# Kernel tuning notes

Hardware: AMD Instinct MI355X
Metric: run time of the kernel (lower is better)

## Reference

```python
import jax, jax.numpy as jnp
import numpy as np

B, N, FN, FE, OUT = 64, 128, 64, 16, 128
S, VOCAB, EMB, LH = 1033, 1033, 50, 8
MOMO, SIDE, T = 200, 963, 3
LN_EPS, BN_EPS = 1e-12, 1e-5


def setup_inputs():
    key = jax.random.key(0)
    ks = iter(jax.random.split(key, 64))
    def nrm(shape, scale=0.05):
        return jax.random.normal(next(ks), shape, dtype=jnp.float32) * scale
    inp = {}
    inp['adjacency_1'] = (jax.random.uniform(next(ks), (B, N, N)) < 0.1).astype(jnp.float32)
    inp['nodes_1'] = nrm((B, N, FN), 1.0)
    inp['edges_1'] = nrm((B, N, N, FE), 1.0)
    inp['adjacency_2'] = (jax.random.uniform(next(ks), (B, N, N)) < 0.1).astype(jnp.float32)
    inp['nodes_2'] = nrm((B, N, FN), 1.0)
    inp['edges_2'] = nrm((B, N, N, FE), 1.0)
    inp['d1_momo_fts'] = nrm((B, MOMO), 1.0)
    inp['d2_momo_fts'] = nrm((B, MOMO), 1.0)
    inp['d1_protein_fts'] = jax.random.randint(next(ks), (B, S), 0, VOCAB)
    inp['d2_protein_fts'] = jax.random.randint(next(ks), (B, S), 0, VOCAB)
    inp['side_effect'] = nrm((B, SIDE), 1.0)
    inp['word_emb'] = nrm((VOCAB, EMB))
    inp['pos_emb'] = nrm((VOCAB, EMB))
    inp['ln_gamma'] = jnp.ones((EMB,), jnp.float32)
    inp['ln_beta'] = jnp.zeros((EMB,), jnp.float32)
    inp['W_ih'] = nrm((4 * LH, EMB))
    inp['W_hh'] = nrm((4 * LH, LH))
    inp['b_ih'] = jnp.zeros((4 * LH,), jnp.float32)
    inp['b_hh'] = jnp.zeros((4 * LH,), jnp.float32)
    inp['dec_W1'] = nrm((LH * S, 256))
    inp['dec_b1'] = jnp.zeros((256,), jnp.float32)
    inp['bn_gamma'] = jnp.ones((256,), jnp.float32)
    inp['bn_beta'] = jnp.zeros((256,), jnp.float32)
    inp['dec_W2'] = nrm((256, 45))
    inp['dec_b2'] = jnp.zeros((45,), jnp.float32)
    for g in ('1', '2'):
        inp['W_msg' + g] = nrm((FN, FN))
        inp['W_edge' + g] = nrm((FE, FN))
        inp['W_up' + g] = nrm((2 * FN, FN))
        inp['b_up' + g] = jnp.zeros((FN,), jnp.float32)
        inp['W_read' + g] = nrm((2 * FN, OUT))
        inp['b_read' + g] = jnp.zeros((OUT,), jnp.float32)
    inp['W_momo'] = nrm((MOMO, 45))
    inp['b_momo'] = jnp.zeros((45,), jnp.float32)
    inp['W_side'] = nrm((SIDE, 32))
    inp['b_side'] = jnp.zeros((32,), jnp.float32)
    inp['W_final'] = nrm((2 * (OUT + 45 + 45) + 32, 1))
    inp['b_final'] = jnp.zeros((1,), jnp.float32)
    return inp


def _mpnn(adj, nodes, edges, W_msg, W_edge, W_up, b_up, W_read, b_read):
    # Dense-masked equivalent of the padded neighbor/edge gather construction:
    # message[b,n] = sum_m adj[b,n,m] * (h[b,m] @ W_msg + e[b,n,m] @ W_edge)
    node_mask = adj.sum(-1) > 0  # [B,N] -- only connected nodes are updated
    edge_msg = jnp.einsum('bnm,bnmf,fk->bnk', adj, edges, W_edge)  # static over passes
    h = nodes
    for _ in range(T):
        msg = jnp.einsum('bnm,bmf,fk->bnk', adj, h, W_msg) + edge_msg
        upd = jax.nn.relu(jnp.concatenate([h, msg], -1) @ W_up + b_up)
        h = jnp.where(node_mask[..., None], upd, h)
    r = jax.nn.relu(jnp.concatenate([h, nodes], -1) @ W_read + b_read)  # [B,N,OUT]
    return jnp.einsum('bn,bnk->bk', node_mask.astype(h.dtype), r)


def _protein(ids, word_emb, pos_emb, ln_gamma, ln_beta, W_ih, W_hh, b_ih, b_hh,
             dec_W1, dec_b1, bn_gamma, bn_beta, dec_W2, dec_b2):
    x = word_emb[ids] + pos_emb[jnp.arange(S)][None]  # [B,S,EMB]
    u = x.mean(-1, keepdims=True)
    s = ((x - u) ** 2).mean(-1, keepdims=True)
    x = ln_gamma * (x - u) / jnp.sqrt(s + LN_EPS) + ln_beta
    def step(carry, xt):  # torch LSTM gate order: i, f, g, o
        h, c = carry
        gates = xt @ W_ih.T + b_ih + h @ W_hh.T + b_hh
        i, f, g, o = jnp.split(gates, 4, axis=-1)
        c = jax.nn.sigmoid(f) * c + jax.nn.sigmoid(i) * jnp.tanh(g)
        h = jax.nn.sigmoid(o) * jnp.tanh(c)
        return (h, c), h
    h0 = jnp.zeros((ids.shape[0], LH), jnp.float32)
    _, hs = jax.lax.scan(step, (h0, h0), jnp.swapaxes(x, 0, 1))  # [S,B,LH]
    p = jnp.swapaxes(hs, 0, 1).reshape(ids.shape[0], -1)  # [B, S*LH]
    p = jax.nn.relu(p @ dec_W1 + dec_b1)
    m, v = p.mean(0), p.var(0)  # BatchNorm1d in training mode (batch stats)
    p = bn_gamma * (p - m) / jnp.sqrt(v + BN_EPS) + bn_beta
    return p @ dec_W2 + dec_b2  # [B,45]


def reference(adjacency_1, nodes_1, edges_1, adjacency_2, nodes_2, edges_2,
              d1_momo_fts, d1_protein_fts, d2_momo_fts, d2_protein_fts, side_effect,
              word_emb, pos_emb, ln_gamma, ln_beta, W_ih, W_hh, b_ih, b_hh,
              dec_W1, dec_b1, bn_gamma, bn_beta, dec_W2, dec_b2,
              W_msg1, W_edge1, W_up1, b_up1, W_read1, b_read1,
              W_msg2, W_edge2, W_up2, b_up2, W_read2, b_read2,
              W_momo, b_momo, W_side, b_side, W_final, b_final):
    out1 = _mpnn(adjacency_1, nodes_1, edges_1, W_msg1, W_edge1, W_up1, b_up1, W_read1, b_read1)
    out2 = _mpnn(adjacency_2, nodes_2, edges_2, W_msg2, W_edge2, W_up2, b_up2, W_read2, b_read2)
    p1 = _protein(d1_protein_fts, word_emb, pos_emb, ln_gamma, ln_beta, W_ih, W_hh, b_ih, b_hh,
                  dec_W1, dec_b1, bn_gamma, bn_beta, dec_W2, dec_b2)
    p2 = _protein(d2_protein_fts, word_emb, pos_emb, ln_gamma, ln_beta, W_ih, W_hh, b_ih, b_hh,
                  dec_W1, dec_b1, bn_gamma, bn_beta, dec_W2, dec_b2)
    momo1 = d1_momo_fts @ W_momo + b_momo
    momo2 = d2_momo_fts @ W_momo + b_momo
    drug1 = jnp.concatenate([out1, p1, momo1], axis=1)
    drug2 = jnp.concatenate([out2, p2, momo2], axis=1)
    side = side_effect @ W_side + b_side
    feats = jnp.concatenate([drug1, drug2, side], axis=1)
    return feats @ W_final + b_final  # [B,1]
```

## Files before the change

kernel.cpp:

```cpp
#include <hip/hip_runtime.h>
#include <hip/hip_bf16.h>
#include <math.h>

#define Bb 64
#define Nn 128
#define FNf 64
#define Ss 1033
#define EMBe 50

typedef float f4 __attribute__((ext_vector_type(4)));
typedef float f2 __attribute__((ext_vector_type(2)));
typedef int   i4 __attribute__((ext_vector_type(4)));

#define HS_KSTRIDE 1036
#define HS_BSTRIDE 8288
#define HS_PSIZE   530432

constexpr size_t OFF_EMSG  = 2*524288 + 2*524288;
constexpr size_t OFF_MASK  = OFF_EMSG  + 2*524288;
constexpr size_t OFF_OUT12 = OFF_MASK  + 2*8192;
constexpr size_t OFF_PPRE  = OFF_OUT12 + 2*8192;
constexpr size_t OFF_PBN   = OFF_PPRE  + 2*16384;
constexpr size_t OFF_XW    = OFF_PBN   + 2*16384;
constexpr size_t OFF_HS    = OFF_XW    + 2*2115584;
constexpr size_t OFF_W2F   = OFF_HS    + 2*HS_PSIZE;
constexpr size_t OFF_WMF   = OFF_W2F   + 2*256;
constexpr size_t OFF_WSF   = OFF_WMF   + 2*200;
constexpr size_t OFF_CONST = OFF_WSF   + 964;
constexpr size_t OFF_COUNT = OFF_CONST + 4;
constexpr size_t OFF_NZ    = OFF_COUNT + 2*8192;
constexpr size_t OFF_AVAL  = OFF_NZ    + 2*524288;

__device__ inline f4 relu4(f4 v) {
  v[0] = fmaxf(v[0], 0.f); v[1] = fmaxf(v[1], 0.f);
  v[2] = fmaxf(v[2], 0.f); v[3] = fmaxf(v[3], 0.f);
  return v;
}

#define ROR16(x, n) __int_as_float(__builtin_amdgcn_update_dpp(0, __float_as_int(x), 0x120 + (n), 0xF, 0xF, true))

__global__ __launch_bounds__(256) void kA(
    const float* __restrict__ adj1, const float* __restrict__ adj2,
    const float* __restrict__ edges1, const float* __restrict__ edges2,
    const float* __restrict__ We1, const float* __restrict__ We2,
    const int* __restrict__ ids1, const int* __restrict__ ids2,
    const float* __restrict__ we, const float* __restrict__ pe,
    const float* __restrict__ lng, const float* __restrict__ lnb,
    const float* __restrict__ Wih, const float* __restrict__ bih,
    const float* __restrict__ bhh, float* __restrict__ ws) {
  int bid = blockIdx.x;
  int t = threadIdx.x;
  if (bid < 4096) {
    int g = bid >> 11;
    int w = t >> 6, lane = t & 63;
    int row = (bid & 2047) * 4 + w;
    const float* adj   = g ? adj2 : adj1;
    const float* edges = g ? edges2 : edges1;
    const float* We    = g ? We2 : We1;
    float* emsg  = ws + OFF_EMSG + (size_t)g * 524288;
    int*   cntg  = (int*)(ws + OFF_COUNT) + (size_t)g * 8192;
    int*   nz    = (int*)(ws + OFF_NZ)    + (size_t)g * 524288;
    float* aval  = ws + OFF_AVAL + (size_t)g * 524288;

    __shared__ int   lidx[4][64];
    __shared__ float lav[4][64];
    __shared__ float les[4][16];

    const float* arow = adj + (size_t)row * 128;
    float a0 = arow[lane], a1 = arow[64 + lane];
    unsigned long long m0 = __ballot(a0 != 0.f);
    unsigned long long m1 = __ballot(a1 != 0.f);
    int c0 = __popcll(m0);
    int cnt = c0 + __popcll(m1);
    unsigned long long below = ((unsigned long long)1 << lane) - 1ull;
    if (a0 != 0.f) { int pos = __popcll(m0 & below); if (pos < 64) { lidx[w][pos] = lane; lav[w][pos] = a0; } }
    if (a1 != 0.f) { int pos = c0 + __popcll(m1 & below); if (pos < 64) { lidx[w][pos] = lane + 64; lav[w][pos] = a1; } }
    int cc = cnt > 64 ? 64 : cnt;
    __syncthreads();

    nz[(size_t)row * 64 + lane]   = (lane < cc) ? lidx[w][lane] : 0;
    aval[(size_t)row * 64 + lane] = (lane < cc) ? lav[w][lane] : 0.f;

    int f = lane & 15, js = lane >> 4;
    float es = 0.f;
    const float* erow = edges + (size_t)row * 128 * 16;
    for (int j = js; j < cc; j += 4) es += lav[w][j] * erow[lidx[w][j] * 16 + f];
    es += __shfl_xor(es, 16);
    es += __shfl_xor(es, 32);
    if (lane < 16) les[w][lane] = es;
    __syncthreads();

    float acc = 0.f;
    #pragma unroll
    for (int ff = 0; ff < 16; ++ff) acc += les[w][ff] * We[ff * 64 + lane];
    emsg[(size_t)row * 64 + lane] = acc;
    if (lane == 0) cntg[row] = cc;
    return;
  }
  int bid6 = bid - 4096;
  int p = bid6 / 2066;
  int xb = bid6 % 2066;
  const int* ids = p ? ids2 : ids1;
  float* xw = ws + OFF_XW + (size_t)p * 2115584;
  __shared__ float wlds[1600];
  __shared__ float glds[50], blds[50], bs[32];
  __shared__ float xl6[8][52];
  for (int i = t; i < 1600; i += 256) wlds[i] = Wih[i];
  if (t < 50) { glds[t] = lng[t]; blds[t] = lnb[t]; }
  if (t < 32) bs[t] = bih[t] + bhh[t];
  __syncthreads();
  int grp = t >> 5, tl = t & 31;
  int newpos = (tl < 16) ? 2 * tl : 2 * tl - 31;
  const float L = 1.44269504088896f;
  float scale = (tl >= 16 && tl < 24) ? -2.f * L : -L;
  int q0 = xb * 32 + grp * 4;
  for (int qq = 0; qq < 4; ++qq) {
    int q = q0 + qq;
    int s = q % Ss;
    int id = ids[q];
    const float* wr = we + (size_t)id * 50;
    const float* pr = pe + (size_t)s * 50;
    float x1 = wr[tl] + pr[tl];
    bool has2 = (tl + 32) < 50;
    float x2 = has2 ? (wr[tl + 32] + pr[tl + 32]) : 0.f;
    float sm = x1 + x2, sq = x1 * x1 + x2 * x2;
    #pragma unroll
    for (int off = 16; off; off >>= 1) {
      sm += __shfl_xor(sm, off, 32);
      sq += __shfl_xor(sq, off, 32);
    }
    float u = sm * (1.f / 50.f);
    float var = fmaxf(sq * (1.f / 50.f) - u * u, 0.f);
    float rstd = rsqrtf(var + 1e-12f);
    xl6[grp][tl] = glds[tl] * (x1 - u) * rstd + blds[tl];
    if (has2) xl6[grp][tl + 32] = glds[tl + 32] * (x2 - u) * rstd + blds[tl + 32];
    __syncthreads();
    float acc = bs[tl];
    #pragma unroll 10
    for (int k = 0; k < 50; ++k) acc += xl6[grp][k] * wlds[tl * 50 + k];
    xw[(size_t)q * 32 + newpos] = acc * scale;
    __syncthreads();
  }
}

__global__ __launch_bounds__(256) void kB(
    const float* __restrict__ nodes1, const float* __restrict__ nodes2,
    const float* __restrict__ Wm1, const float* __restrict__ Wm2,
    const float* __restrict__ Wup1, const float* __restrict__ Wup2,
    const float* __restrict__ bup1, const float* __restrict__ bup2,
    const float* __restrict__ Wr1, const float* __restrict__ Wr2,
    const float* __restrict__ br1, const float* __restrict__ br2,
    const float* __restrict__ Whh, float* __restrict__ ws) {
  __shared__ __attribute__((aligned(16))) float hl[8192];
  __shared__ __attribute__((aligned(16))) float xl[8192];
  __shared__ __attribute__((aligned(16))) float wml[4096];
  __shared__ __attribute__((aligned(16))) float wbl[8192];
  int bid = blockIdx.x;
  int t = threadIdx.x;
  if (bid >= 128) {
    if (t >= 64) return;
    int idx = bid - 128;
    int p = idx >> 4, xb = idx & 15;
    const float* xw = ws + OFF_XW + (size_t)p * 2115584;
    float* hs = ws + OFF_HS + (size_t)p * HS_PSIZE;
    int lane16 = t & 15;
    int k = lane16 & 7;
    int half = lane16 >> 3;
    int b = xb * 4 + (t >> 4);
    const float* xwp = xw + (size_t)b * (Ss * 32) + lane16 * 2;
    float* hq = hs + (size_t)b * HS_BSTRIDE + (size_t)k * HS_KSTRIDE;
    const float L = 1.44269504088896f;
    int ga = half ? 8 + k : k;
    int gb = half ? 24 + k : 16 + k;
    float sb_scale = half ? -L : -2.f * L;
    float wa[8], wb[8];
    #pragma unroll
    for (int r = 0; r < 8; ++r) {
      int j = (k - r) & 7;
      wa[r] = -L * Whh[ga * 8 + j];
      wb[r] = sb_scale * Whh[gb * 8 + j];
    }
    float A = half ? 0.f : -4.f * L;
    float B = half ? 1.f : 2.f * L;
    float ho = 0.f, cs = 0.f;
    float q0v = 0.f, q1v = 0.f, q2v = 0.f, q3v = 0.f;

    f2 x[8];
    #pragma unroll
    for (int j = 0; j < 8; ++j) x[j] = *(const f2*)(xwp + (size_t)j * 32);
    const float* pf = xwp + 8 * 32;

    auto step = [&](f2 xc) {
      float h1 = ROR16(ho, 1);
      float h2 = ROR16(ho, 2);
      float h3 = ROR16(ho, 3);
      float h4 = ROR16(ho, 4);
      float h5 = ROR16(ho, 5);
      float h6 = ROR16(ho, 6);
      float h7 = ROR16(ho, 7);
      float a0 = fmaf(ho, wa[0], xc.x);
      float b0 = fmaf(ho, wb[0], xc.y);
      a0 = fmaf(h1, wa[1], a0);  b0 = fmaf(h1, wb[1], b0);
      a0 = fmaf(h2, wa[2], a0);  b0 = fmaf(h2, wb[2], b0);
      a0 = fmaf(h3, wa[3], a0);  b0 = fmaf(h3, wb[3], b0);
      float a1 = h4 * wa[4];     float b1 = h4 * wb[4];
      a1 = fmaf(h5, wa[5], a1);  b1 = fmaf(h5, wb[5], b1);
      a1 = fmaf(h6, wa[6], a1);  b1 = fmaf(h6, wb[6], b1);
      a1 = fmaf(h7, wa[7], a1);  b1 = fmaf(h7, wb[7], b1);
      float acc_a = a0 + a1;
      float acc_b = b0 + b1;
      float ea = __builtin_amdgcn_exp2f(acc_a);
      float sa = __builtin_amdgcn_rcpf(1.f + ea);
      float eb = __builtin_amdgcn_exp2f(acc_b);
      float tb = __builtin_amdgcn_rcpf(1.f + eb);
      float x_own = fmaf(sa * A, tb, sa * B);
      float x_oth = ROR16(x_own, 8);
      float t_oth = ROR16(tb, 8);
      float F  = half ? x_own : x_oth;
      float P2 = half ? x_oth : x_own;
      cs = fmaf(F, cs, P2);
      float e2 = __builtin_amdgcn_exp2f(cs);
      float tc = __builtin_amdgcn_rcpf(1.f + e2);
      float so = half ? tb : t_oth;
      ho = fmaf(so + so, tc, -so);
    };

    for (int g = 0; g < 129; ++g) {
      #pragma unroll
      for (int j = 0; j < 8; ++j) {
        f2 xc = x[j];
        x[j] = *(const f2*)(pf + j * 32);
        step(xc);
        if (j == 0 || j == 4) q0v = ho;
        else if (j == 1 || j == 5) q1v = ho;
        else if (j == 2 || j == 6) q2v = ho;
        else if (j == 3) { q3v = ho; if (!half) *(f4*)(hq + 0) = (f4){q0v, q1v, q2v, q3v}; }
        else { q3v = ho; if (!half) *(f4*)(hq + 4) = (f4){q0v, q1v, q2v, q3v}; }
      }
      pf += 256;
      hq += 8;
    }
    step(x[0]);
    if (!half) hq[0] = ho;
    return;
  }
  int g = bid >> 6, b = bid & 63;
  const float* nodes = g ? nodes2 : nodes1;
  const float* Wm  = g ? Wm2 : Wm1;
  const float* Wup = g ? Wup2 : Wup1;
  const float* bup = g ? bup2 : bup1;
  const float* Wr  = g ? Wr2 : Wr1;
  const float* br  = g ? br2 : br1;
  const float* emsg = ws + OFF_EMSG + (size_t)g * 524288;
  const int*   cntg = (const int*)(ws + OFF_COUNT) + (size_t)g * 8192;
  const int*   nz   = (const int*)(ws + OFF_NZ) + (size_t)g * 524288;
  const float* aval = ws + OFF_AVAL + (size_t)g * 524288;
  float* out12 = ws + OFF_OUT12 + (size_t)g * 8192;

  int col4 = (t & 15) * 4, rg = t >> 4;
  int r0 = rg * 8;
  for (int i = t; i < 4096; i += 256) wml[i] = Wm[i];
  for (int i = t; i < 8192; i += 256) wbl[i] = Wup[i];
  for (int i = t; i < 8192; i += 256) hl[i] = nodes[(size_t)b * 8192 + i];
  __syncthreads();

  for (int it = 0; it < 3; ++it) {
    {
      f4 acc[8];
      #pragma unroll
      for (int rr = 0; rr < 8; ++rr) acc[rr] = (f4){0.f, 0.f, 0.f, 0.f};
      for (int f0 = 0; f0 < 64; f0 += 4) {
        f4 h4[8];
        #pragma unroll
        for (int rr = 0; rr < 8; ++rr) h4[rr] = *(const f4*)&hl[(r0 + rr) * 64 + f0];
        #pragma unroll
        for (int ff = 0; ff < 4; ++ff) {
          f4 w4 = *(const f4*)&wml[(f0 + ff) * 64 + col4];
          #pragma unroll
          for (int rr = 0; rr < 8; ++rr) acc[rr] += h4[rr][ff] * w4;
        }
      }
      #pragma unroll
      for (int rr = 0; rr < 8; ++rr) *(f4*)&xl[(r0 + rr) * 64 + col4] = acc[rr];
    }
    __syncthreads();
    f4 msgv[8];
    #pragma unroll
    for (int rr = 0; rr < 8; ++rr) {
      int row = b * 128 + r0 + rr;
      f4 m = *(const f4*)&emsg[(size_t)row * 64 + col4];
      int cnt4 = (cntg[row] + 3) >> 2;
      const i4* nzr = (const i4*)(nz + (size_t)row * 64);
      const f4* avr = (const f4*)(aval + (size_t)row * 64);
      for (int j4 = 0; j4 < cnt4; ++j4) {
        i4 nq = nzr[j4];
        f4 aq = avr[j4];
        m += aq[0] * *(const f4*)&xl[nq[0] * 64 + col4];
        m += aq[1] * *(const f4*)&xl[nq[1] * 64 + col4];
        m += aq[2] * *(const f4*)&xl[nq[2] * 64 + col4];
        m += aq[3] * *(const f4*)&xl[nq[3] * 64 + col4];
      }
      msgv[rr] = m;
    }
    __syncthreads();
    #pragma unroll
    for (int rr = 0; rr < 8; ++rr) *(f4*)&xl[(r0 + rr) * 64 + col4] = msgv[rr];
    __syncthreads();
    {
      f4 u[8];
      #pragma unroll
      for (int rr = 0; rr < 8; ++rr) u[rr] = *(const f4*)&bup[col4];
      for (int f0 = 0; f0 < 64; f0 += 4) {
        f4 h4[8];
        #pragma unroll
        for (int rr = 0; rr < 8; ++rr) h4[rr] = *(const f4*)&hl[(r0 + rr) * 64 + f0];
        #pragma unroll
        for (int ff = 0; ff < 4; ++ff) {
          f4 w4 = *(const f4*)&wbl[(f0 + ff) * 64 + col4];
          #pragma unroll
          for (int rr = 0; rr < 8; ++rr) u[rr] += h4[rr][ff] * w4;
        }
      }
      for (int f0 = 0; f0 < 64; f0 += 4) {
        f4 m4[8];
        #pragma unroll
        for (int rr = 0; rr < 8; ++rr) m4[rr] = *(const f4*)&xl[(r0 + rr) * 64 + f0];
        #pragma unroll
        for (int ff = 0; ff < 4; ++ff) {
          f4 w4 = *(const f4*)&wbl[(64 + f0 + ff) * 64 + col4];
          #pragma unroll
          for (int rr = 0; rr < 8; ++rr) u[rr] += m4[rr][ff] * w4;
        }
      }
      __syncthreads();
      #pragma unroll
      for (int rr = 0; rr < 8; ++rr) {
        int row = b * 128 + r0 + rr;
        if (cntg[row] > 0) *(f4*)&hl[(r0 + rr) * 64 + col4] = relu4(u[rr]);
      }
    }
    __syncthreads();
  }

  for (int i = t; i < 8192; i += 256) xl[i] = nodes[(size_t)b * 8192 + i];
  __syncthreads();
  for (int kt = 0; kt < 2; ++kt) {
    for (int i = t; i < 8192; i += 256) {
      int f = i >> 6, c = i & 63;
      wbl[i] = Wr[f * 128 + kt * 64 + c];
    }
    __syncthreads();
    f4 part = {0.f, 0.f, 0.f, 0.f};
    {
      f4 u[8];
      #pragma unroll
      for (int rr = 0; rr < 8; ++rr) u[rr] = *(const f4*)&br[kt * 64 + col4];
      for (int f0 = 0; f0 < 64; f0 += 4) {
        f4 h4[8];
        #pragma unroll
        for (int rr = 0; rr < 8; ++rr) h4[rr] = *(const f4*)&hl[(r0 + rr) * 64 + f0];
        #pragma unroll
        for (int ff = 0; ff < 4; ++ff) {
          f4 w4 = *(const f4*)&wbl[(f0 + ff) * 64 + col4];
          #pragma unroll
          for (int rr = 0; rr < 8; ++rr) u[rr] += h4[rr][ff] * w4;
        }
      }
      for (int f0 = 0; f0 < 64; f0 += 4) {
        f4 n4[8];
        #pragma unroll
        for (int rr = 0; rr < 8; ++rr) n4[rr] = *(const f4*)&xl[(r0 + rr) * 64 + f0];
        #pragma unroll
        for (int ff = 0; ff < 4; ++ff) {
          f4 w4 = *(const f4*)&wbl[(64 + f0 + ff) * 64 + col4];
          #pragma unroll
          for (int rr = 0; rr < 8; ++rr) u[rr] += n4[rr][ff] * w4;
        }
      }
      #pragma unroll
      for (int rr = 0; rr < 8; ++rr) {
        int row = b * 128 + r0 + rr;
        if (cntg[row] > 0) part += relu4(u[rr]);
      }
    }
    *(f4*)&wml[rg * 64 + col4] = part;
    __syncthreads();
    for (int off = 8; off; off >>= 1) {
      if (rg < off) {
        f4 v = *(f4*)&wml[rg * 64 + col4] + *(f4*)&wml[(rg + off) * 64 + col4];
        *(f4*)&wml[rg * 64 + col4] = v;
      }
      __syncthreads();
    }
    if (rg == 0) *(f4*)&out12[(size_t)b * 128 + kt * 64 + col4] = *(f4*)&wml[col4];
    __syncthreads();
  }
}

__global__ __launch_bounds__(256) void kC(
    const float* __restrict__ W1,
    const float* __restrict__ W2, const float* __restrict__ b2,
    const float* __restrict__ Wm, const float* __restrict__ bm,
    const float* __restrict__ Wsd, const float* __restrict__ bsd,
    const float* __restrict__ Wf, const float* __restrict__ bf,
    float* __restrict__ ws) {
  int bid = blockIdx.x;
  int t = threadIdx.x;
  if (bid < 256) {
    int ks = bid & 31, jt = (bid >> 5) & 3, p = bid >> 7;
    const float* hs = ws + OFF_HS + (size_t)p * HS_PSIZE;
    float* pp = ws + OFF_PPRE + (size_t)p * 16384;
    int s0 = ks * 33;
    int s1 = s0 + 33; if (s1 > Ss) s1 = Ss;
    int j0 = jt * 64;
    __shared__ __attribute__((aligned(16))) float hsl[512];
    __shared__ __attribute__((aligned(16))) float w1l[512];
    int jl = (t & 15) * 4, bb = (t >> 4) * 4;
    f4 acc[4] = {};
    for (int s = s0; s < s1; ++s) {
      int i2 = 2 * t;
      hsl[i2]     = hs[(size_t)(i2 >> 3) * HS_BSTRIDE + (size_t)(i2 & 7) * HS_KSTRIDE + s];
      hsl[i2 + 1] = hs[(size_t)((i2 + 1) >> 3) * HS_BSTRIDE + (size_t)((i2 + 1) & 7) * HS_KSTRIDE + s];
      w1l[t]       = W1[(size_t)(s * 8 + (t >> 6)) * 256 + j0 + (t & 63)];
      w1l[t + 256] = W1[(size_t)(s * 8 + ((t + 256) >> 6)) * 256 + j0 + ((t + 256) & 63)];
      __syncthreads();
      #pragma unroll
      for (int l = 0; l < 8; ++l) {
        f4 wv = *(const f4*)&w1l[l * 64 + jl];
        #pragma unroll
        for (int i = 0; i < 4; ++i) acc[i] += hsl[(bb + i) * 8 + l] * wv;
      }
      __syncthreads();
    }
    for (int i = 0; i < 4; ++i) {
      float* dst = pp + (size_t)(bb + i) * 256 + j0 + jl;
      atomicAdd(dst + 0, acc[i][0]); atomicAdd(dst + 1, acc[i][1]);
      atomicAdd(dst + 2, acc[i][2]); atomicAdd(dst + 3, acc[i][3]);
    }
    return;
  }
  __shared__ float wf[468];
  for (int i = t; i < 468; i += 256) wf[i] = Wf[i];
  __syncthreads();
  float* w2f = ws + OFF_W2F;
  float* wmf = ws + OFF_WMF;
  float* wsf = ws + OFF_WSF;
  float* cst = ws + OFF_CONST;
  {
    float a1 = 0.f, a2 = 0.f;
    for (int k = 0; k < 45; ++k) {
      float v = W2[t * 45 + k];
      a1 += v * wf[128 + k];
      a2 += v * wf[346 + k];
    }
    w2f[t] = a1; w2f[256 + t] = a2;
  }
  if (t < 200) {
    float a1 = 0.f, a2 = 0.f;
    for (int k = 0; k < 45; ++k) {
      float v = Wm[t * 45 + k];
      a1 += v * wf[173 + k];
      a2 += v * wf[391 + k];
    }
    wmf[t] = a1; wmf[200 + t] = a2;
  }
  for (int i = t; i < 963; i += 256) {
    float a = 0.f;
    for (int k = 0; k < 32; ++k) a += Wsd[i * 32 + k] * wf[436 + k];
    wsf[i] = a;
  }
  if (t == 0) {
    float cc = bf[0];
    for (int k = 0; k < 45; ++k)
      cc += b2[k] * (wf[128 + k] + wf[346 + k]) + bm[k] * (wf[173 + k] + wf[391 + k]);
    for (int k = 0; k < 32; ++k) cc += bsd[k] * wf[436 + k];
    cst[0] = cc;
  }
}

__global__ __launch_bounds__(256) void kD(
    const float* __restrict__ b1, const float* __restrict__ bng,
    const float* __restrict__ bnb,
    const float* __restrict__ d1m, const float* __restrict__ d2m,
    const float* __restrict__ se, const float* __restrict__ Wf,
    float* __restrict__ ws, float* __restrict__ out) {
  int b = blockIdx.x, t = threadIdx.x;
  const float* out12 = ws + OFF_OUT12;
  const float* pp0 = ws + OFF_PPRE;
  const float* pp1 = ws + OFF_PPRE + 16384;
  const float* w2f = ws + OFF_W2F;
  const float* wmf = ws + OFF_WMF;
  const float* wsf = ws + OFF_WSF;
  float bj = b1[t];
  float sm0 = 0.f, sq0 = 0.f, sm1 = 0.f, sq1 = 0.f;
  for (int bb = 0; bb < 64; ++bb) {
    float v0 = fmaxf(pp0[bb * 256 + t] + bj, 0.f);
    float v1 = fmaxf(pp1[bb * 256 + t] + bj, 0.f);
    sm0 += v0; sq0 += v0 * v0;
    sm1 += v1; sq1 += v1 * v1;
  }
  float m0 = sm0 * (1.f / 64.f);
  float var0 = fmaxf(sq0 * (1.f / 64.f) - m0 * m0, 0.f);
  float rstd0 = rsqrtf(var0 + 1e-5f);
  float sc0 = bng[t] * rstd0, sh0 = bnb[t] - m0 * sc0;
  float m1 = sm1 * (1.f / 64.f);
  float var1 = fmaxf(sq1 * (1.f / 64.f) - m1 * m1, 0.f);
  float rstd1 = rsqrtf(var1 + 1e-5f);
  float sc1 = bng[t] * rstd1, sh1 = bnb[t] - m1 * sc1;
  float val0 = sc0 * fmaxf(pp0[b * 256 + t] + bj, 0.f) + sh0;
  float val1 = sc1 * fmaxf(pp1[b * 256 + t] + bj, 0.f) + sh1;
  float acc = val0 * w2f[t] + val1 * w2f[256 + t];
  if (t < 128) {
    acc += out12[b * 128 + t] * Wf[t];
    acc += out12[8192 + b * 128 + t] * Wf[218 + t];
  }
  if (t < 200) {
    acc += d1m[b * 200 + t] * wmf[t];
    acc += d2m[b * 200 + t] * wmf[200 + t];
  }
  for (int i = t; i < 963; i += 256) acc += se[b * 963 + i] * wsf[i];
  __shared__ float red[256];
  red[t] = acc;
  __syncthreads();
  for (int off = 128; off; off >>= 1) {
    if (t < off) red[t] += red[t + off];
    __syncthreads();
  }
  if (t == 0) out[b] = red[0] + (ws + OFF_CONST)[0];
}

extern "C" void kernel_launch(void* const* d_in, const int* in_sizes, int n_in,
                              void* d_out, int out_size, void* d_ws, size_t ws_size,
                              hipStream_t stream) {
  const float* adj1  = (const float*)d_in[0];
  const float* nodes1= (const float*)d_in[1];
  const float* edges1= (const float*)d_in[2];
  const float* adj2  = (const float*)d_in[3];
  const float* nodes2= (const float*)d_in[4];
  const float* edges2= (const float*)d_in[5];
  const float* d1m   = (const float*)d_in[6];
  const float* d2m   = (const float*)d_in[7];
  const int*   ids1  = (const int*)d_in[8];
  const int*   ids2  = (const int*)d_in[9];
  const float* se    = (const float*)d_in[10];
  const float* we    = (const float*)d_in[11];
  const float* pe    = (const float*)d_in[12];
  const float* lng   = (const float*)d_in[13];
  const float* lnb   = (const float*)d_in[14];
  const float* Wih   = (const float*)d_in[15];
  const float* Whh   = (const float*)d_in[16];
  const float* bih   = (const float*)d_in[17];
  const float* bhh   = (const float*)d_in[18];
  const float* W1    = (const float*)d_in[19];
  const float* b1    = (const float*)d_in[20];
  const float* bng   = (const float*)d_in[21];
  const float* bnb   = (const float*)d_in[22];
  const float* W2    = (const float*)d_in[23];
  const float* b2    = (const float*)d_in[24];
  const float* Wm1   = (const float*)d_in[25];
  const float* We1   = (const float*)d_in[26];
  const float* Wup1  = (const float*)d_in[27];
  const float* bup1  = (const float*)d_in[28];
  const float* Wr1   = (const float*)d_in[29];
  const float* br1   = (const float*)d_in[30];
  const float* Wm2   = (const float*)d_in[31];
  const float* We2   = (const float*)d_in[32];
  const float* Wup2  = (const float*)d_in[33];
  const float* bup2  = (const float*)d_in[34];
  const float* Wr2   = (const float*)d_in[35];
  const float* br2   = (const float*)d_in[36];
  const float* Wmo   = (const float*)d_in[37];
  const float* bmo   = (const float*)d_in[38];
  const float* Wsd   = (const float*)d_in[39];
  const float* bsd   = (const float*)d_in[40];
  const float* Wf    = (const float*)d_in[41];
  const float* bf    = (const float*)d_in[42];
  float* ws = (float*)d_ws;
  float* out = (float*)d_out;

  hipMemsetAsync(ws + OFF_PPRE, 0, 2 * 16384 * sizeof(float), stream);

  kA<<<8228, 256, 0, stream>>>(adj1, adj2, edges1, edges2, We1, We2,
                               ids1, ids2, we, pe, lng, lnb, Wih, bih, bhh, ws);
  kB<<<160, 256, 0, stream>>>(nodes1, nodes2, Wm1, Wm2, Wup1, Wup2, bup1, bup2,
                              Wr1, Wr2, br1, br2, Whh, ws);
  kC<<<257, 256, 0, stream>>>(W1, W2, b2, Wmo, bmo, Wsd, bsd, Wf, bf, ws);
  kD<<<64, 256, 0, stream>>>(b1, bng, bnb, d1m, d2m, se, Wf, ws, out);
}
```

Baseline: 237.8 us.

## Store LSTM hidden states time-major and batch multiple timesteps in decoder GEMM

The LSTM recurrence now writes its hidden state for each timestep into a time-major buffer, with all batch and hidden values contiguous for each step. The decoder first-layer kernel can then load each step's 512 values with coalesced vector loads, instead of gathering strided scalars from the old per-batch, per-k padded layout. That kernel also stages three timesteps per barrier pair with padded shared rows and vector register reads, cutting the number of block barriers. The embedding kernel replaces its block-wide barriers with wave barriers, which is only correct if each group's shared buffer is touched by a single wavefront. The recurrence now issues scalar stores with a large stride instead of packed f4 stores, which may cost more in that serial loop.

```diff
diff --git a/kernel.cpp b/kernel.cpp
--- a/kernel.cpp
+++ b/kernel.cpp
@@ -12,9 +12,7 @@
 typedef float f2 __attribute__((ext_vector_type(2)));
 typedef int   i4 __attribute__((ext_vector_type(4)));
 
-#define HS_KSTRIDE 1036
-#define HS_BSTRIDE 8288
-#define HS_PSIZE   530432
+#define HS_PSIZE 528896
 
 constexpr size_t OFF_EMSG  = 2*524288 + 2*524288;
 constexpr size_t OFF_MASK  = OFF_EMSG  + 2*524288;
@@ -134,12 +132,12 @@
     float rstd = rsqrtf(var + 1e-12f);
     xl6[grp][tl] = glds[tl] * (x1 - u) * rstd + blds[tl];
     if (has2) xl6[grp][tl + 32] = glds[tl + 32] * (x2 - u) * rstd + blds[tl + 32];
-    __syncthreads();
+    __builtin_amdgcn_wave_barrier();
     float acc = bs[tl];
     #pragma unroll 10
     for (int k = 0; k < 50; ++k) acc += xl6[grp][k] * wlds[tl * 50 + k];
     xw[(size_t)q * 32 + newpos] = acc * scale;
-    __syncthreads();
+    __builtin_amdgcn_wave_barrier();
   }
 }
 
@@ -168,7 +166,7 @@
     int half = lane16 >> 3;
     int b = xb * 4 + (t >> 4);
     const float* xwp = xw + (size_t)b * (Ss * 32) + lane16 * 2;
-    float* hq = hs + (size_t)b * HS_BSTRIDE + (size_t)k * HS_KSTRIDE;
+    float* hq = hs + (size_t)b * 8 + k;
     const float L = 1.44269504088896f;
     int ga = half ? 8 + k : k;
     int gb = half ? 24 + k : 16 + k;
@@ -183,7 +181,6 @@
     float A = half ? 0.f : -4.f * L;
     float B = half ? 1.f : 2.f * L;
     float ho = 0.f, cs = 0.f;
-    float q0v = 0.f, q1v = 0.f, q2v = 0.f, q3v = 0.f;
 
     f2 x[8];
     #pragma unroll
@@ -231,17 +228,13 @@
         f2 xc = x[j];
         x[j] = *(const f2*)(pf + j * 32);
         step(xc);
-        if (j == 0 || j == 4) q0v = ho;
-        else if (j == 1 || j == 5) q1v = ho;
-        else if (j == 2 || j == 6) q2v = ho;
-        else if (j == 3) { q3v = ho; if (!half) *(f4*)(hq + 0) = (f4){q0v, q1v, q2v, q3v}; }
-        else { q3v = ho; if (!half) *(f4*)(hq + 4) = (f4){q0v, q1v, q2v, q3v}; }
+        if (!half) *hq = ho;
+        hq += 512;
       }
       pf += 256;
-      hq += 8;
     }
     step(x[0]);
-    if (!half) hq[0] = ho;
+    if (!half) *hq = ho;
     return;
   }
   int g = bid >> 6, b = bid & 63;
@@ -413,27 +406,49 @@
     int s0 = ks * 33;
     int s1 = s0 + 33; if (s1 > Ss) s1 = Ss;
     int j0 = jt * 64;
-    __shared__ __attribute__((aligned(16))) float hsl[512];
-    __shared__ __attribute__((aligned(16))) float w1l[512];
-    int jl = (t & 15) * 4, bb = (t >> 4) * 4;
+    __shared__ __attribute__((aligned(16))) float hsl[3][64 * 12];
+    __shared__ __attribute__((aligned(16))) float w1l[3][512];
+    int jl = (t & 15) * 4, bb = t >> 4;
     f4 acc[4] = {};
-    for (int s = s0; s < s1; ++s) {
-      int i2 = 2 * t;
-      hsl[i2]     = hs[(size_t)(i2 >> 3) * HS_BSTRIDE + (size_t)(i2 & 7) * HS_KSTRIDE + s];
-      hsl[i2 + 1] = hs[(size_t)((i2 + 1) >> 3) * HS_BSTRIDE + (size_t)((i2 + 1) & 7) * HS_KSTRIDE + s];
-      w1l[t]       = W1[(size_t)(s * 8 + (t >> 6)) * 256 + j0 + (t & 63)];
-      w1l[t + 256] = W1[(size_t)(s * 8 + ((t + 256) >> 6)) * 256 + j0 + ((t + 256) & 63)];
+    int wb = (2 * t) & 7;
+    int wbrow = t >> 2;
+    for (int sb = s0; sb < s1; sb += 3) {
+      int ns = s1 - sb; if (ns > 3) ns = 3;
+      for (int ss = 0; ss < ns; ++ss) {
+        int s = sb + ss;
+        f2 v = *(const f2*)&hs[(size_t)s * 512 + 2 * t];
+        *(f2*)&hsl[ss][wbrow * 12 + wb] = v;
+        if (t < 128) {
+          *(f4*)&w1l[ss][(t >> 4) * 64 + (t & 15) * 4] =
+              *(const f4*)&W1[(size_t)(s * 8 + (t >> 4)) * 256 + j0 + (t & 15) * 4];
+        }
+      }
       __syncthreads();
-      #pragma unroll
-      for (int l = 0; l < 8; ++l) {
-        f4 wv = *(const f4*)&w1l[l * 64 + jl];
-        #pragma unroll
-        for (int i = 0; i < 4; ++i) acc[i] += hsl[(bb + i) * 8 + l] * wv;
+      for (int ss = 0; ss < 3; ++ss) {
+        if (ss >= ns) break;
+        f4 r[4][2];
+        #pragma unroll
+        for (int i = 0; i < 4; ++i) {
+          int b = bb + 16 * i;
+          r[i][0] = *(const f4*)&hsl[ss][b * 12];
+          r[i][1] = *(const f4*)&hsl[ss][b * 12 + 4];
+        }
+        #pragma unroll
+        for (int l = 0; l < 8; ++l) {
+          f4 wv = *(const f4*)&w1l[ss][l * 64 + jl];
+          #pragma unroll
+          for (int i = 0; i < 4; ++i) {
+            float hv = (l < 4) ? r[i][0][l] : r[i][1][l - 4];
+            acc[i] += hv * wv;
+          }
+        }
       }
       __syncthreads();
     }
+    #pragma unroll
     for (int i = 0; i < 4; ++i) {
-      float* dst = pp + (size_t)(bb + i) * 256 + j0 + jl;
+      int b = bb + 16 * i;
+      float* dst = pp + (size_t)b * 256 + j0 + jl;
       atomicAdd(dst + 0, acc[i][0]); atomicAdd(dst + 1, acc[i][1]);
       atomicAdd(dst + 2, acc[i][2]); atomicAdd(dst + 3, acc[i][3]);
     }
```

Measured after the change: 249.2 us. 1.05x slower.
